# Kernel optimization log

Hardware: AMD Instinct MI355X
Metric: run time of the kernel (lower is better)

## Reference

```python
import jax, jax.numpy as jnp
import numpy as np

NUM_HEADS = 12
MODEL_SIZE = 768
HEAD_SIZE = MODEL_SIZE // NUM_HEADS
DIM = 768


def setup_inputs() -> dict:
    key = jax.random.key(0)
    ks = jax.random.split(key, 11)
    B, S, D = 4, 2048, MODEL_SIZE
    scale = 0.02
    return {
        "query": jax.random.normal(ks[0], (B, S, D), jnp.float32),
        "key": jax.random.normal(ks[1], (B, S, D), jnp.float32),
        "value": jax.random.normal(ks[2], (B, S, D), jnp.float32),
        "wq": jax.random.normal(ks[3], (D, MODEL_SIZE), jnp.float32) * scale,
        "bq": jnp.zeros((MODEL_SIZE,), jnp.float32),
        "wk": jax.random.normal(ks[4], (D, MODEL_SIZE), jnp.float32) * scale,
        "bk": jnp.zeros((MODEL_SIZE,), jnp.float32),
        "wv": jax.random.normal(ks[5], (D, MODEL_SIZE), jnp.float32) * scale,
        "bv": jnp.zeros((MODEL_SIZE,), jnp.float32),
        "wo": jax.random.normal(ks[6], (MODEL_SIZE, DIM), jnp.float32) * scale,
        "bo": jnp.zeros((DIM,), jnp.float32),
    }


def _split_heads(x):
    # [B, S, model_size] -> [B, H, S, head_size]
    B, S, _ = x.shape
    return x.reshape(B, S, NUM_HEADS, HEAD_SIZE).transpose(0, 2, 1, 3)


def reference(query, key, value, wq, bq, wk, bk, wv, bv, wo, bo):
    q = _split_heads(query @ wq + bq)   # [B,H,S,d]
    k = _split_heads(key @ wk + bk)
    v = _split_heads(value @ wv + bv)
    scale = 1.0 / jnp.sqrt(jnp.float32(HEAD_SIZE))
    score = jnp.einsum('bhqd,bhkd->bhqk', q, k) * scale
    alpha = jax.nn.softmax(score, axis=-1)
    ctx = jnp.einsum('bhqk,bhkd->bhqd', alpha, v)
    B, H, S, d = ctx.shape
    ctx = ctx.transpose(0, 2, 1, 3).reshape(B, S, H * d)
    # Dropout(0.2) is inference-mode (identity) in the original call
    return ctx @ wo + bo
```

## Files before the change

### kernel.cpp

```cpp
#include <hip/hip_runtime.h>
#include <stdint.h>

#define DEV static __device__ __forceinline__

typedef unsigned short u16;
typedef __attribute__((ext_vector_type(8))) short s16x8;
typedef __attribute__((ext_vector_type(4))) float f32x4;

DEV u16 f2bf(float x) {
    uint32_t u = __float_as_uint(x);
    u = u + 0x7FFFu + ((u >> 16) & 1u);
    return (u16)(u >> 16);
}
DEV u16 f2bf_trunc(float x) {
    return (u16)(__float_as_uint(x) >> 16);
}

DEV f32x4 mfma_bf16(s16x8 a, s16x8 b, f32x4 c) {
    return __builtin_amdgcn_mfma_f32_16x16x32_bf16(a, b, c, 0, 0, 0);
}

constexpr int Bq   = 4;
constexpr int S    = 2048;
constexpr int D    = 768;
constexpr int H    = 12;
constexpr int HD   = 64;
constexpr int BS   = Bq * S;
constexpr float SC_LOG2 = 0.18033688011112042f;

__global__ __launch_bounds__(256) void k_wtrans(const float* __restrict__ w0, const float* __restrict__ w1,
                                                const float* __restrict__ w2, const float* __restrict__ w3,
                                                u16* __restrict__ t0, u16* __restrict__ t1,
                                                u16* __restrict__ t2, u16* __restrict__ t3) {
    const float* w = (blockIdx.z == 0) ? w0 : (blockIdx.z == 1) ? w1 : (blockIdx.z == 2) ? w2 : w3;
    u16*         t = (blockIdx.z == 0) ? t0 : (blockIdx.z == 1) ? t1 : (blockIdx.z == 2) ? t2 : t3;
    __shared__ float tile[64 * 65];
    const int k0 = blockIdx.y * 64, n0 = blockIdx.x * 64;
    const int tx = threadIdx.x & 15, ty = threadIdx.x >> 4;
#pragma unroll
    for (int rr = 0; rr < 4; rr++) {
        int kl = rr * 16 + ty;
        float4 v = *(const float4*)&w[(size_t)(k0 + kl) * D + n0 + tx * 4];
        tile[kl * 65 + tx * 4 + 0] = v.x;
        tile[kl * 65 + tx * 4 + 1] = v.y;
        tile[kl * 65 + tx * 4 + 2] = v.z;
        tile[kl * 65 + tx * 4 + 3] = v.w;
    }
    __syncthreads();
#pragma unroll
    for (int rr = 0; rr < 4; rr++) {
        int nl = rr * 16 + ty;
        int kl = tx * 4;
        ushort4 o = make_ushort4(f2bf(tile[(kl + 0) * 65 + nl]), f2bf(tile[(kl + 1) * 65 + nl]),
                                 f2bf(tile[(kl + 2) * 65 + nl]), f2bf(tile[(kl + 3) * 65 + nl]));
        *(ushort4*)&t[(size_t)(n0 + nl) * D + k0 + kl] = o;
    }
}

struct GemmArgs { const void* A; const u16* BT; const float* bias; void* dst; };
struct GemmArgs3 { GemmArgs g[3]; };

DEV int4 pack8(float4 a, float4 b) {
    int4 r;
    r.x = (int)((uint32_t)f2bf(a.x) | ((uint32_t)f2bf(a.y) << 16));
    r.y = (int)((uint32_t)f2bf(a.z) | ((uint32_t)f2bf(a.w) << 16));
    r.z = (int)((uint32_t)f2bf(b.x) | ((uint32_t)f2bf(b.y) << 16));
    r.w = (int)((uint32_t)f2bf(b.z) | ((uint32_t)f2bf(b.w) << 16));
    return r;
}

template <int MODE, bool AF32>
__global__ __launch_bounds__(256, 2) void k_gemm(GemmArgs3 args) {
    const GemmArgs& G = args.g[blockIdx.y];
    const u16* __restrict__ BT = G.BT;
    const float* __restrict__ bias = G.bias;

    __shared__ __align__(16) char smem[36864];
    u16* As = (u16*)smem;
    u16* Bs = (u16*)(smem + 128 * 72 * 2);
    const int tid = threadIdx.x;
    const int lane = tid & 63;
    const int w = tid >> 6, wm = w >> 1, wn = w & 1;
    const int l16 = lane & 15, lg = lane >> 4;
    const int mtile = (int)blockIdx.x / 6, ntile = (int)blockIdx.x % 6;
    const int m0 = mtile * 128, n0 = ntile * 128;

    const int sr = tid >> 3, sp = tid & 7;

    f32x4 acc[4][4];
#pragma unroll
    for (int i = 0; i < 4; i++)
#pragma unroll
        for (int j = 0; j < 4; j++) acc[i][j] = f32x4{0.f, 0.f, 0.f, 0.f};

    int4 ar[4], br[4];
    auto load = [&](int k0) {
#pragma unroll
        for (int i = 0; i < 4; i++) {
            if (AF32) {
                const float* Af = (const float*)G.A;
                float4 x = *(const float4*)&Af[(size_t)(m0 + sr + i * 32) * D + k0 + sp * 8];
                float4 y = *(const float4*)&Af[(size_t)(m0 + sr + i * 32) * D + k0 + sp * 8 + 4];
                ar[i] = pack8(x, y);
            } else {
                ar[i] = *(const int4*)&((const u16*)G.A)[(size_t)(m0 + sr + i * 32) * D + k0 + sp * 8];
            }
            br[i] = *(const int4*)&BT[(size_t)(n0 + sr + i * 32) * D + k0 + sp * 8];
        }
    };
    load(0);
    for (int t = 0; t < 12; t++) {
        __syncthreads();
#pragma unroll
        for (int i = 0; i < 4; i++) {
            *(int4*)&As[(sr + i * 32) * 72 + sp * 8] = ar[i];
            *(int4*)&Bs[(sr + i * 32) * 72 + sp * 8] = br[i];
        }
        __syncthreads();
        if (t < 11) load((t + 1) * 64);
#pragma unroll
        for (int kk = 0; kk < 2; kk++) {
            s16x8 af[4], bf[4];
#pragma unroll
            for (int mf = 0; mf < 4; mf++)
                af[mf] = *(const s16x8*)&As[(wm * 64 + mf * 16 + l16) * 72 + kk * 32 + lg * 8];
#pragma unroll
            for (int nf = 0; nf < 4; nf++)
                bf[nf] = *(const s16x8*)&Bs[(wn * 64 + nf * 16 + l16) * 72 + kk * 32 + lg * 8];
#pragma unroll
            for (int mf = 0; mf < 4; mf++)
#pragma unroll
                for (int nf = 0; nf < 4; nf++) acc[mf][nf] = mfma_bf16(af[mf], bf[nf], acc[mf][nf]);
        }
    }
    __syncthreads();
    if (MODE == 0) {
        u16* Cs = (u16*)smem;
#pragma unroll
        for (int nf = 0; nf < 4; nf++) {
            float bv = bias[n0 + wn * 64 + nf * 16 + l16];
#pragma unroll
            for (int mf = 0; mf < 4; mf++)
#pragma unroll
                for (int rg = 0; rg < 4; rg++)
                    Cs[(wm * 64 + mf * 16 + lg * 4 + rg) * 136 + wn * 64 + nf * 16 + l16] =
                        f2bf(acc[mf][nf][rg] + bv);
        }
        __syncthreads();
#pragma unroll
        for (int i = 0; i < 8; i++) {
            int idx = i * 256 + tid;
            int row = idx >> 4, ch = idx & 15;
            int gm = m0 + row;
            int b = gm >> 11, s = gm & 2047;
            int c = ch * 8;
            int h = (n0 + c) >> 6, dd = c & 63;
            int4 v = *(const int4*)&Cs[row * 136 + c];
            *(int4*)&((u16*)G.dst)[(size_t)((b * H + h) * S + s) * HD + dd] = v;
        }
    } else {
        float* Cf = (float*)smem;
#pragma unroll
        for (int p = 0; p < 2; p++) {
            if (wm == p) {
#pragma unroll
                for (int nf = 0; nf < 4; nf++) {
                    float bv = bias[n0 + wn * 64 + nf * 16 + l16];
#pragma unroll
                    for (int mf = 0; mf < 4; mf++)
#pragma unroll
                        for (int rg = 0; rg < 4; rg++)
                            Cf[(mf * 16 + lg * 4 + rg) * 132 + wn * 64 + nf * 16 + l16] =
                                acc[mf][nf][rg] + bv;
                }
            }
            __syncthreads();
#pragma unroll
            for (int i = 0; i < 8; i++) {
                int idx = i * 256 + tid;
                int row = idx >> 5, ch = idx & 31;
                float4 v = *(const float4*)&Cf[row * 132 + ch * 4];
                *(float4*)&((float*)G.dst)[(size_t)(m0 + p * 64 + row) * D + n0 + ch * 4] = v;
            }
            if (p == 0) __syncthreads();
        }
    }
}

__global__ __launch_bounds__(256) void k_vtrans(const u16* __restrict__ Vh, u16* __restrict__ VT) {
    __shared__ u16 t[64 * 70];
    const int bh = blockIdx.y, s0 = blockIdx.x * 64;
    const u16* src = Vh + (size_t)bh * S * HD;
    u16* dst = VT + (size_t)bh * HD * S;
    const int tx = threadIdx.x & 15, ty = threadIdx.x >> 4;
#pragma unroll
    for (int rr = 0; rr < 4; rr++) {
        int sl = rr * 16 + ty;
        ushort4 v = *(const ushort4*)&src[(size_t)(s0 + sl) * HD + tx * 4];
        t[sl * 70 + tx * 4 + 0] = v.x;
        t[sl * 70 + tx * 4 + 1] = v.y;
        t[sl * 70 + tx * 4 + 2] = v.z;
        t[sl * 70 + tx * 4 + 3] = v.w;
    }
    __syncthreads();
#pragma unroll
    for (int rr = 0; rr < 4; rr++) {
        int dl = rr * 16 + ty;
        int sl = tx * 4;
        ushort4 o = make_ushort4(t[(sl + 0) * 70 + dl], t[(sl + 1) * 70 + dl],
                                 t[(sl + 2) * 70 + dl], t[(sl + 3) * 70 + dl]);
        *(ushort4*)&dst[(size_t)dl * S + s0 + sl] = o;
    }
}

__global__ __launch_bounds__(512, 2) void k_attn(const u16* __restrict__ Qh,
                                                 const u16* __restrict__ Kh,
                                                 const u16* __restrict__ VT,
                                                 u16* __restrict__ CTX) {
    __shared__ u16 Ks[64 * 72];
    __shared__ u16 Vs[64 * 72];
    __shared__ u16 Ps[8][32 * 72];
    const int tid = threadIdx.x, lane = tid & 63, w = tid >> 6;
    const int l16 = lane & 15, lg = lane >> 4;
    const int bh = blockIdx.y;
    const int q0 = blockIdx.x * 256 + w * 32;
    const u16* Qb = Qh + (size_t)bh * S * HD;
    const u16* Kb = Kh + (size_t)bh * S * HD;
    const u16* Vb = VT + (size_t)bh * HD * S;
    u16* Pw = &Ps[w][0];

    s16x8 qf[2][2];
#pragma unroll
    for (int mf = 0; mf < 2; mf++)
#pragma unroll
        for (int kk = 0; kk < 2; kk++)
            qf[mf][kk] = *(const s16x8*)&Qb[(size_t)(q0 + mf * 16 + l16) * HD + kk * 32 + lg * 8];

    f32x4 o[2][5];
#pragma unroll
    for (int mf = 0; mf < 2; mf++)
#pragma unroll
        for (int nf = 0; nf < 5; nf++) o[mf][nf] = f32x4{0.f, 0.f, 0.f, 0.f};

    const s16x8 ones = {0x3F80, 0x3F80, 0x3F80, 0x3F80, 0x3F80, 0x3F80, 0x3F80, 0x3F80};

    const int sr = tid >> 3, sp = tid & 7;
    int4 krg, vrg;
    auto loadkv = [&](int kv0) {
        krg = *(const int4*)&Kb[(size_t)(kv0 + sr) * HD + sp * 8];
        vrg = *(const int4*)&Vb[(size_t)sr * S + kv0 + sp * 8];
    };
    loadkv(0);
    for (int t = 0; t < S / 64; t++) {
        __syncthreads();
        *(int4*)&Ks[sr * 72 + sp * 8] = krg;
        *(int4*)&Vs[sr * 72 + sp * 8] = vrg;
        __syncthreads();
        if (t < S / 64 - 1) loadkv((t + 1) * 64);

        f32x4 sc[2][4];
#pragma unroll
        for (int mf = 0; mf < 2; mf++)
#pragma unroll
            for (int nf = 0; nf < 4; nf++) sc[mf][nf] = f32x4{0.f, 0.f, 0.f, 0.f};
#pragma unroll
        for (int kk = 0; kk < 2; kk++) {
#pragma unroll
            for (int nf = 0; nf < 4; nf++) {
                s16x8 kf = *(const s16x8*)&Ks[(nf * 16 + l16) * 72 + kk * 32 + lg * 8];
                sc[0][nf] = mfma_bf16(qf[0][kk], kf, sc[0][nf]);
                sc[1][nf] = mfma_bf16(qf[1][kk], kf, sc[1][nf]);
            }
        }
#pragma unroll
        for (int mf = 0; mf < 2; mf++)
#pragma unroll
            for (int nf = 0; nf < 4; nf++)
#pragma unroll
                for (int rg = 0; rg < 4; rg++) {
                    float p = __builtin_amdgcn_exp2f(sc[mf][nf][rg] * SC_LOG2);
                    Pw[(mf * 16 + lg * 4 + rg) * 72 + nf * 16 + l16] = f2bf_trunc(p);
                }
#pragma unroll
        for (int kk = 0; kk < 2; kk++) {
            s16x8 pf[2];
#pragma unroll
            for (int mf = 0; mf < 2; mf++)
                pf[mf] = *(const s16x8*)&Pw[(mf * 16 + l16) * 72 + kk * 32 + lg * 8];
#pragma unroll
            for (int nf = 0; nf < 4; nf++) {
                s16x8 vf = *(const s16x8*)&Vs[(nf * 16 + l16) * 72 + kk * 32 + lg * 8];
                o[0][nf] = mfma_bf16(pf[0], vf, o[0][nf]);
                o[1][nf] = mfma_bf16(pf[1], vf, o[1][nf]);
            }
            o[0][4] = mfma_bf16(pf[0], ones, o[0][4]);
            o[1][4] = mfma_bf16(pf[1], ones, o[1][4]);
        }
    }
    const int b = bh / H, h = bh - b * H;
#pragma unroll
    for (int mf = 0; mf < 2; mf++)
#pragma unroll
        for (int rg = 0; rg < 4; rg++) {
            int gq = q0 + mf * 16 + lg * 4 + rg;
            float inv = 1.0f / o[mf][4][rg];
#pragma unroll
            for (int nf = 0; nf < 4; nf++) {
                int dc = nf * 16 + l16;
                CTX[(size_t)(b * S + gq) * D + h * HD + dc] = f2bf(o[mf][nf][rg] * inv);
            }
        }
}

extern "C" void kernel_launch(void* const* d_in, const int* in_sizes, int n_in,
                              void* d_out, int out_size, void* d_ws, size_t ws_size,
                              hipStream_t stream) {
    const float* query = (const float*)d_in[0];
    const float* key   = (const float*)d_in[1];
    const float* value = (const float*)d_in[2];
    const float* wq    = (const float*)d_in[3];
    const float* bq    = (const float*)d_in[4];
    const float* wk    = (const float*)d_in[5];
    const float* bk    = (const float*)d_in[6];
    const float* wv    = (const float*)d_in[7];
    const float* bv    = (const float*)d_in[8];
    const float* wo    = (const float*)d_in[9];
    const float* bo    = (const float*)d_in[10];

    char* ws = (char*)d_ws;
    constexpr size_t SZ_ACT = (size_t)BS * D * 2;
    constexpr size_t SZ_W   = (size_t)D * D * 2;
    u16* wqT = (u16*)(ws);
    u16* wkT = (u16*)(ws + 1 * SZ_W);
    u16* wvT = (u16*)(ws + 2 * SZ_W);
    u16* woT = (u16*)(ws + 3 * SZ_W);
    char* base2 = ws + 4 * SZ_W;
    u16* Qhp = (u16*)(base2);
    u16* Khp = (u16*)(base2 + SZ_ACT);
    u16* Vhp = (u16*)(base2 + 2 * SZ_ACT);
    u16* VTp = (u16*)(base2 + 3 * SZ_ACT);
    u16* CTX = (u16*)(base2 + 4 * SZ_ACT);

    (void)in_sizes; (void)n_in; (void)out_size; (void)ws_size;

    k_wtrans<<<dim3(D / 64, D / 64, 4), 256, 0, stream>>>(wq, wk, wv, wo, wqT, wkT, wvT, woT);

    GemmArgs3 qkv;
    qkv.g[0] = {query, wqT, bq, Qhp};
    qkv.g[1] = {key,   wkT, bk, Khp};
    qkv.g[2] = {value, wvT, bv, Vhp};
    k_gemm<0, true><<<dim3((BS / 128) * (D / 128), 3), 256, 0, stream>>>(qkv);

    k_vtrans<<<dim3(S / 64, Bq * H), 256, 0, stream>>>(Vhp, VTp);
    k_attn<<<dim3(S / 256, Bq * H), 512, 0, stream>>>(Qhp, Khp, VTp, CTX);

    GemmArgs3 outa;
    outa.g[0] = {CTX, woT, bo, d_out};
    outa.g[1] = outa.g[0];
    outa.g[2] = outa.g[0];
    k_gemm<1, false><<<dim3((BS / 128) * (D / 128), 1), 256, 0, stream>>>(outa);
}
```

Baseline: 423.1 us.

## Pre-convert fp32 inputs to bf16 and swizzle block order across XCDs

A separate kernel now converts the fp32 query/key/value activations to bf16 before the QKV GEMM, so the GEMM loads half the bytes per A tile and does no conversion in its inner loop, at the cost of an extra pass over memory. The GEMM and attention grids are flattened and remapped with an XCD-aware swizzle (blocks with the same low 3 bits grouped) so that neighbouring tiles that share data run on the same XCD and L2. GEMM launch bounds are raised to 3 blocks per SM, and the CTX buffer reuses the bf16 query buffer.

```diff
diff --git a/kernel.cpp b/kernel.cpp
--- a/kernel.cpp
+++ b/kernel.cpp
@@ -19,6 +19,8 @@
 DEV f32x4 mfma_bf16(s16x8 a, s16x8 b, f32x4 c) {
     return __builtin_amdgcn_mfma_f32_16x16x32_bf16(a, b, c, 0, 0, 0);
 }
+
+DEV int swz8(int bid, int nwg) { return (bid & 7) * (nwg >> 3) + (bid >> 3); }
 
 constexpr int Bq   = 4;
 constexpr int S    = 2048;
@@ -27,6 +29,29 @@
 constexpr int HD   = 64;
 constexpr int BS   = Bq * S;
 constexpr float SC_LOG2 = 0.18033688011112042f;
+
+DEV int4 pack8(float4 a, float4 b) {
+    int4 r;
+    r.x = (int)((uint32_t)f2bf(a.x) | ((uint32_t)f2bf(a.y) << 16));
+    r.y = (int)((uint32_t)f2bf(a.z) | ((uint32_t)f2bf(a.w) << 16));
+    r.z = (int)((uint32_t)f2bf(b.x) | ((uint32_t)f2bf(b.y) << 16));
+    r.w = (int)((uint32_t)f2bf(b.z) | ((uint32_t)f2bf(b.w) << 16));
+    return r;
+}
+
+__global__ __launch_bounds__(256) void k_conv(const float* __restrict__ q,
+                                              const float* __restrict__ k,
+                                              const float* __restrict__ v,
+                                              u16* __restrict__ dq,
+                                              u16* __restrict__ dk,
+                                              u16* __restrict__ dv) {
+    const float* s = (blockIdx.y == 0) ? q : (blockIdx.y == 1) ? k : v;
+    u16*         d = (blockIdx.y == 0) ? dq : (blockIdx.y == 1) ? dk : dv;
+    size_t i = ((size_t)blockIdx.x * 256 + threadIdx.x) * 8;
+    float4 x = *(const float4*)&s[i];
+    float4 y = *(const float4*)&s[i + 4];
+    *(int4*)&d[i] = pack8(x, y);
+}
 
 __global__ __launch_bounds__(256) void k_wtrans(const float* __restrict__ w0, const float* __restrict__ w1,
                                                 const float* __restrict__ w2, const float* __restrict__ w3,
@@ -57,21 +82,17 @@
     }
 }
 
-struct GemmArgs { const void* A; const u16* BT; const float* bias; void* dst; };
+struct GemmArgs { const u16* A; const u16* BT; const float* bias; void* dst; };
 struct GemmArgs3 { GemmArgs g[3]; };
 
-DEV int4 pack8(float4 a, float4 b) {
-    int4 r;
-    r.x = (int)((uint32_t)f2bf(a.x) | ((uint32_t)f2bf(a.y) << 16));
-    r.y = (int)((uint32_t)f2bf(a.z) | ((uint32_t)f2bf(a.w) << 16));
-    r.z = (int)((uint32_t)f2bf(b.x) | ((uint32_t)f2bf(b.y) << 16));
-    r.w = (int)((uint32_t)f2bf(b.z) | ((uint32_t)f2bf(b.w) << 16));
-    return r;
-}
-
-template <int MODE, bool AF32>
-__global__ __launch_bounds__(256, 2) void k_gemm(GemmArgs3 args) {
-    const GemmArgs& G = args.g[blockIdx.y];
+template <int MODE>
+__global__ __launch_bounds__(256, 3) void k_gemm(GemmArgs3 args) {
+    const int f = swz8((int)blockIdx.x, (int)gridDim.x);
+    const int gy = f / 384;
+    const int r = f - gy * 384;
+    const int mtile = r / 6, ntile = r % 6;
+    const GemmArgs& G = args.g[gy];
+    const u16* __restrict__ A  = G.A;
     const u16* __restrict__ BT = G.BT;
     const float* __restrict__ bias = G.bias;
 
@@ -82,7 +103,6 @@
     const int lane = tid & 63;
     const int w = tid >> 6, wm = w >> 1, wn = w & 1;
     const int l16 = lane & 15, lg = lane >> 4;
-    const int mtile = (int)blockIdx.x / 6, ntile = (int)blockIdx.x % 6;
     const int m0 = mtile * 128, n0 = ntile * 128;
 
     const int sr = tid >> 3, sp = tid & 7;
@@ -97,14 +117,7 @@
     auto load = [&](int k0) {
 #pragma unroll
         for (int i = 0; i < 4; i++) {
-            if (AF32) {
-                const float* Af = (const float*)G.A;
-                float4 x = *(const float4*)&Af[(size_t)(m0 + sr + i * 32) * D + k0 + sp * 8];
-                float4 y = *(const float4*)&Af[(size_t)(m0 + sr + i * 32) * D + k0 + sp * 8 + 4];
-                ar[i] = pack8(x, y);
-            } else {
-                ar[i] = *(const int4*)&((const u16*)G.A)[(size_t)(m0 + sr + i * 32) * D + k0 + sp * 8];
-            }
+            ar[i] = *(const int4*)&A[(size_t)(m0 + sr + i * 32) * D + k0 + sp * 8];
             br[i] = *(const int4*)&BT[(size_t)(n0 + sr + i * 32) * D + k0 + sp * 8];
         }
     };
@@ -222,8 +235,9 @@
     __shared__ u16 Ps[8][32 * 72];
     const int tid = threadIdx.x, lane = tid & 63, w = tid >> 6;
     const int l16 = lane & 15, lg = lane >> 4;
-    const int bh = blockIdx.y;
-    const int q0 = blockIdx.x * 256 + w * 32;
+    const int f = swz8((int)blockIdx.x, (int)gridDim.x);
+    const int bh = f >> 3;
+    const int q0 = (f & 7) * 256 + w * 32;
     const u16* Qb = Qh + (size_t)bh * S * HD;
     const u16* Kb = Kh + (size_t)bh * S * HD;
     const u16* Vb = VT + (size_t)bh * HD * S;
@@ -335,28 +349,32 @@
     u16* wvT = (u16*)(ws + 2 * SZ_W);
     u16* woT = (u16*)(ws + 3 * SZ_W);
     char* base2 = ws + 4 * SZ_W;
-    u16* Qhp = (u16*)(base2);
-    u16* Khp = (u16*)(base2 + SZ_ACT);
-    u16* Vhp = (u16*)(base2 + 2 * SZ_ACT);
-    u16* VTp = (u16*)(base2 + 3 * SZ_ACT);
-    u16* CTX = (u16*)(base2 + 4 * SZ_ACT);
+    u16* qbf = (u16*)(base2);
+    u16* kbf = (u16*)(base2 + SZ_ACT);
+    u16* vbf = (u16*)(base2 + 2 * SZ_ACT);
+    u16* Qhp = (u16*)(base2 + 3 * SZ_ACT);
+    u16* Khp = (u16*)(base2 + 4 * SZ_ACT);
+    u16* Vhp = (u16*)(base2 + 5 * SZ_ACT);
+    u16* VTp = (u16*)(base2 + 6 * SZ_ACT);
+    u16* CTX = qbf;
 
     (void)in_sizes; (void)n_in; (void)out_size; (void)ws_size;
 
+    k_conv<<<dim3(BS * D / 8 / 256, 3), 256, 0, stream>>>(query, key, value, qbf, kbf, vbf);
     k_wtrans<<<dim3(D / 64, D / 64, 4), 256, 0, stream>>>(wq, wk, wv, wo, wqT, wkT, wvT, woT);
 
     GemmArgs3 qkv;
-    qkv.g[0] = {query, wqT, bq, Qhp};
-    qkv.g[1] = {key,   wkT, bk, Khp};
-    qkv.g[2] = {value, wvT, bv, Vhp};
-    k_gemm<0, true><<<dim3((BS / 128) * (D / 128), 3), 256, 0, stream>>>(qkv);
+    qkv.g[0] = {qbf, wqT, bq, Qhp};
+    qkv.g[1] = {kbf, wkT, bk, Khp};
+    qkv.g[2] = {vbf, wvT, bv, Vhp};
+    k_gemm<0><<<dim3(3 * (BS / 128) * (D / 128)), 256, 0, stream>>>(qkv);
 
     k_vtrans<<<dim3(S / 64, Bq * H), 256, 0, stream>>>(Vhp, VTp);
-    k_attn<<<dim3(S / 256, Bq * H), 512, 0, stream>>>(Qhp, Khp, VTp, CTX);
+    k_attn<<<dim3((S / 256) * Bq * H), 512, 0, stream>>>(Qhp, Khp, VTp, CTX);
 
     GemmArgs3 outa;
     outa.g[0] = {CTX, woT, bo, d_out};
     outa.g[1] = outa.g[0];
     outa.g[2] = outa.g[0];
-    k_gemm<1, false><<<dim3((BS / 128) * (D / 128), 1), 256, 0, stream>>>(outa);
-}
+    k_gemm<1><<<dim3((BS / 128) * (D / 128)), 256, 0, stream>>>(outa);
+}
```

New measurement: 432.5 us. +2.2%, slower.

## Fuse V transpose into QKV GEMM epilogue and swizzle block order across XCDs

Applied to the files above, without the earlier changes.

The QKV projection epilogue for the V matrix now writes its tile transposed, directly into the head-major [B,H,HD,S] layout through shared memory. This removes the separate V-transpose kernel and its extra round trip through global memory. The GEMM and attention grids are flattened to 1D and remapped with an 8-way block swizzle so neighbouring tiles land on the same XCD, aiming for better L2 reuse. GEMM launch bounds are raised to 3 blocks per CU, which may raise register pressure or cause spills.

```diff
diff --git a/kernel.cpp b/kernel.cpp
--- a/kernel.cpp
+++ b/kernel.cpp
@@ -19,6 +19,8 @@
 DEV f32x4 mfma_bf16(s16x8 a, s16x8 b, f32x4 c) {
     return __builtin_amdgcn_mfma_f32_16x16x32_bf16(a, b, c, 0, 0, 0);
 }
+
+DEV int swz8(int bid, int nwg) { return (bid & 7) * (nwg >> 3) + (bid >> 3); }
 
 constexpr int Bq   = 4;
 constexpr int S    = 2048;
@@ -27,6 +29,15 @@
 constexpr int HD   = 64;
 constexpr int BS   = Bq * S;
 constexpr float SC_LOG2 = 0.18033688011112042f;
+
+DEV int4 pack8(float4 a, float4 b) {
+    int4 r;
+    r.x = (int)((uint32_t)f2bf(a.x) | ((uint32_t)f2bf(a.y) << 16));
+    r.y = (int)((uint32_t)f2bf(a.z) | ((uint32_t)f2bf(a.w) << 16));
+    r.z = (int)((uint32_t)f2bf(b.x) | ((uint32_t)f2bf(b.y) << 16));
+    r.w = (int)((uint32_t)f2bf(b.z) | ((uint32_t)f2bf(b.w) << 16));
+    return r;
+}
 
 __global__ __launch_bounds__(256) void k_wtrans(const float* __restrict__ w0, const float* __restrict__ w1,
                                                 const float* __restrict__ w2, const float* __restrict__ w3,
@@ -60,18 +71,13 @@
 struct GemmArgs { const void* A; const u16* BT; const float* bias; void* dst; };
 struct GemmArgs3 { GemmArgs g[3]; };
 
-DEV int4 pack8(float4 a, float4 b) {
-    int4 r;
-    r.x = (int)((uint32_t)f2bf(a.x) | ((uint32_t)f2bf(a.y) << 16));
-    r.y = (int)((uint32_t)f2bf(a.z) | ((uint32_t)f2bf(a.w) << 16));
-    r.z = (int)((uint32_t)f2bf(b.x) | ((uint32_t)f2bf(b.y) << 16));
-    r.w = (int)((uint32_t)f2bf(b.z) | ((uint32_t)f2bf(b.w) << 16));
-    return r;
-}
-
 template <int MODE, bool AF32>
-__global__ __launch_bounds__(256, 2) void k_gemm(GemmArgs3 args) {
-    const GemmArgs& G = args.g[blockIdx.y];
+__global__ __launch_bounds__(256, 3) void k_gemm(GemmArgs3 args) {
+    const int f = swz8((int)blockIdx.x, (int)gridDim.x);
+    const int gy = f / 384;
+    const int r = f - gy * 384;
+    const int mtile = r / 6, ntile = r % 6;
+    const GemmArgs& G = args.g[gy];
     const u16* __restrict__ BT = G.BT;
     const float* __restrict__ bias = G.bias;
 
@@ -82,7 +88,6 @@
     const int lane = tid & 63;
     const int w = tid >> 6, wm = w >> 1, wn = w & 1;
     const int l16 = lane & 15, lg = lane >> 4;
-    const int mtile = (int)blockIdx.x / 6, ntile = (int)blockIdx.x % 6;
     const int m0 = mtile * 128, n0 = ntile * 128;
 
     const int sr = tid >> 3, sp = tid & 7;
@@ -134,7 +139,35 @@
         }
     }
     __syncthreads();
-    if (MODE == 0) {
+    if (MODE == 0 && gy == 2) {
+        u16* Ct = (u16*)smem;
+#pragma unroll
+        for (int nf = 0; nf < 4; nf++) {
+            int col = wn * 64 + nf * 16 + l16;
+            float bv = bias[n0 + col];
+#pragma unroll
+            for (int mf = 0; mf < 4; mf++) {
+                int row = wm * 64 + mf * 16 + lg * 4;
+#pragma unroll
+                for (int rp = 0; rp < 2; rp++) {
+                    uint32_t pk = (uint32_t)f2bf(acc[mf][nf][rp * 2] + bv) |
+                                  ((uint32_t)f2bf(acc[mf][nf][rp * 2 + 1] + bv) << 16);
+                    *(uint32_t*)&Ct[col * 136 + row + rp * 2] = pk;
+                }
+            }
+        }
+        __syncthreads();
+        const int b = m0 >> 11, s0 = m0 & 2047;
+#pragma unroll
+        for (int i = 0; i < 8; i++) {
+            int idx = i * 256 + tid;
+            int col = idx >> 4, ch = idx & 15;
+            int gcol = n0 + col;
+            int h = gcol >> 6, dd = gcol & 63;
+            int4 v = *(const int4*)&Ct[col * 136 + ch * 8];
+            *(int4*)&((u16*)G.dst)[((size_t)(b * H + h) * HD + dd) * S + s0 + ch * 8] = v;
+        }
+    } else if (MODE == 0) {
         u16* Cs = (u16*)smem;
 #pragma unroll
         for (int nf = 0; nf < 4; nf++) {
@@ -187,32 +220,6 @@
     }
 }
 
-__global__ __launch_bounds__(256) void k_vtrans(const u16* __restrict__ Vh, u16* __restrict__ VT) {
-    __shared__ u16 t[64 * 70];
-    const int bh = blockIdx.y, s0 = blockIdx.x * 64;
-    const u16* src = Vh + (size_t)bh * S * HD;
-    u16* dst = VT + (size_t)bh * HD * S;
-    const int tx = threadIdx.x & 15, ty = threadIdx.x >> 4;
-#pragma unroll
-    for (int rr = 0; rr < 4; rr++) {
-        int sl = rr * 16 + ty;
-        ushort4 v = *(const ushort4*)&src[(size_t)(s0 + sl) * HD + tx * 4];
-        t[sl * 70 + tx * 4 + 0] = v.x;
-        t[sl * 70 + tx * 4 + 1] = v.y;
-        t[sl * 70 + tx * 4 + 2] = v.z;
-        t[sl * 70 + tx * 4 + 3] = v.w;
-    }
-    __syncthreads();
-#pragma unroll
-    for (int rr = 0; rr < 4; rr++) {
-        int dl = rr * 16 + ty;
-        int sl = tx * 4;
-        ushort4 o = make_ushort4(t[(sl + 0) * 70 + dl], t[(sl + 1) * 70 + dl],
-                                 t[(sl + 2) * 70 + dl], t[(sl + 3) * 70 + dl]);
-        *(ushort4*)&dst[(size_t)dl * S + s0 + sl] = o;
-    }
-}
-
 __global__ __launch_bounds__(512, 2) void k_attn(const u16* __restrict__ Qh,
                                                  const u16* __restrict__ Kh,
                                                  const u16* __restrict__ VT,
@@ -222,8 +229,9 @@
     __shared__ u16 Ps[8][32 * 72];
     const int tid = threadIdx.x, lane = tid & 63, w = tid >> 6;
     const int l16 = lane & 15, lg = lane >> 4;
-    const int bh = blockIdx.y;
-    const int q0 = blockIdx.x * 256 + w * 32;
+    const int f = swz8((int)blockIdx.x, (int)gridDim.x);
+    const int bh = f >> 3;
+    const int q0 = (f & 7) * 256 + w * 32;
     const u16* Qb = Qh + (size_t)bh * S * HD;
     const u16* Kb = Kh + (size_t)bh * S * HD;
     const u16* Vb = VT + (size_t)bh * HD * S;
@@ -337,9 +345,8 @@
     char* base2 = ws + 4 * SZ_W;
     u16* Qhp = (u16*)(base2);
     u16* Khp = (u16*)(base2 + SZ_ACT);
-    u16* Vhp = (u16*)(base2 + 2 * SZ_ACT);
-    u16* VTp = (u16*)(base2 + 3 * SZ_ACT);
-    u16* CTX = (u16*)(base2 + 4 * SZ_ACT);
+    u16* VTp = (u16*)(base2 + 2 * SZ_ACT);
+    u16* CTX = (u16*)(base2 + 3 * SZ_ACT);
 
     (void)in_sizes; (void)n_in; (void)out_size; (void)ws_size;
 
@@ -348,15 +355,14 @@
     GemmArgs3 qkv;
     qkv.g[0] = {query, wqT, bq, Qhp};
     qkv.g[1] = {key,   wkT, bk, Khp};
-    qkv.g[2] = {value, wvT, bv, Vhp};
-    k_gemm<0, true><<<dim3((BS / 128) * (D / 128), 3), 256, 0, stream>>>(qkv);
-
-    k_vtrans<<<dim3(S / 64, Bq * H), 256, 0, stream>>>(Vhp, VTp);
-    k_attn<<<dim3(S / 256, Bq * H), 512, 0, stream>>>(Qhp, Khp, VTp, CTX);
+    qkv.g[2] = {value, wvT, bv, VTp};
+    k_gemm<0, true><<<dim3(3 * (BS / 128) * (D / 128)), 256, 0, stream>>>(qkv);
+
+    k_attn<<<dim3((S / 256) * Bq * H), 512, 0, stream>>>(Qhp, Khp, VTp, CTX);
 
     GemmArgs3 outa;
     outa.g[0] = {CTX, woT, bo, d_out};
     outa.g[1] = outa.g[0];
     outa.g[2] = outa.g[0];
-    k_gemm<1, false><<<dim3((BS / 128) * (D / 128), 1), 256, 0, stream>>>(outa);
-}
+    k_gemm<1, false><<<dim3((BS / 128) * (D / 128)), 256, 0, stream>>>(outa);
+}
```

Measured after the change: 388.7 us. -8.1%, faster.
